# Kernel tuning notes

Measured on AMD Instinct MI355X. Metric: run time of the kernel, lower is better.

The kernel has to match this reference:

```python
import jax, jax.numpy as jnp
import numpy as np

N_ACTIVE = 200000
N_IN = 64
N_OUT = 64
K = 27          # filter volume (3^3)
R = 100000      # rulebook pairs per filter offset


def setup_inputs() -> dict:
    key = jax.random.key(0)
    k1, k2, k3, k4 = jax.random.split(key, 4)
    std = (2.0 / (N_IN * K)) ** 0.5
    features = jax.random.normal(k1, (N_ACTIVE, N_IN), dtype=jnp.float32)
    weight = jax.random.normal(k2, (N_IN * K, N_OUT), dtype=jnp.float32) * std
    bias = jnp.zeros((N_OUT,), dtype=jnp.float32)
    in_idx = jax.random.randint(k3, (K, R), 0, N_ACTIVE, dtype=jnp.int64 if jax.config.jax_enable_x64 else jnp.int32)
    out_idx = jax.random.randint(k4, (K, R), 0, N_ACTIVE, dtype=jnp.int64 if jax.config.jax_enable_x64 else jnp.int32)
    return {"features": features, "weight": weight, "bias": bias,
            "in_idx": in_idx, "out_idx": out_idx}


def reference(features, weight, bias, in_idx, out_idx):
    # Rulebook-based submanifold sparse convolution:
    # for each filter offset k: gather inputs, matmul with weight slice,
    # scatter-accumulate into output sites. Bias added once per active site.
    n_active, n_in = features.shape
    k = in_idx.shape[0]
    W = weight.reshape(k, n_in, -1)            # [K, nIn, nOut]
    gathered = features[in_idx]                # [K, R, nIn]  (irregular gather)
    contrib = jnp.einsum('kri,kio->kro', gathered, W)  # grouped matmul
    out = jnp.zeros((n_active, W.shape[2]), dtype=features.dtype)
    out = out.at[out_idx.reshape(-1)].add(contrib.reshape(-1, W.shape[2]))
    return out + bias
```

## Files before the change

kernel.cpp:

```cpp
#include <hip/hip_runtime.h>
#include <stdint.h>

#define N_ACTIVE 200000
#define N_IN 64
#define N_OUT 64
#define K_FILT 27
#define R_PAIRS 100000
#define TOTP (K_FILT * R_PAIRS)
#define NSLOT (N_ACTIVE * K_FILT)

#define CF_BLOCKS (N_ACTIVE * N_IN / 8 / 256)
#define CW_BLOCKS K_FILT
#define CL_BLOCKS ((TOTP + 255) / 256)

typedef __bf16 bf16x8 __attribute__((ext_vector_type(8)));
typedef float f32x4 __attribute__((ext_vector_type(4)));

__global__ __launch_bounds__(256) void prep_fused(
    const float* __restrict__ feat, __bf16* __restrict__ featb,
    const float* __restrict__ wsrc, __bf16* __restrict__ wt,
    const int* __restrict__ in_idx, const int* __restrict__ out_idx,
    int* __restrict__ slotW,
    int2* __restrict__ ovf, int* __restrict__ ovfCur)
{
    int bb = blockIdx.x, t = threadIdx.x;
    if (bb < CF_BLOCKS) {
        int i = bb * 256 + t;
        const f32x4* src = reinterpret_cast<const f32x4*>(feat) + 2 * (size_t)i;
        f32x4 v0 = __builtin_nontemporal_load(src);
        f32x4 v1 = __builtin_nontemporal_load(src + 1);
        bf16x8 o;
        o[0] = (__bf16)v0[0]; o[1] = (__bf16)v0[1]; o[2] = (__bf16)v0[2]; o[3] = (__bf16)v0[3];
        o[4] = (__bf16)v1[0]; o[5] = (__bf16)v1[1]; o[6] = (__bf16)v1[2]; o[7] = (__bf16)v1[3];
        reinterpret_cast<bf16x8*>(featb)[i] = o;
    } else if (bb < CF_BLOCKS + CW_BLOCKS) {
        int kf = bb - CF_BLOCKS;
        const float* wk = wsrc + kf * 4096;
        __bf16* wo = wt + kf * 4096;
        int o = t >> 2, i0 = (t & 3) * 16;
        bf16x8 a, b;
        #pragma unroll
        for (int j = 0; j < 8; ++j) a[j] = (__bf16)wk[(i0 + j) * 64 + o];
        #pragma unroll
        for (int j = 0; j < 8; ++j) b[j] = (__bf16)wk[(i0 + 8 + j) * 64 + o];
        *reinterpret_cast<bf16x8*>(wo + o * 64 + i0) = a;
        *reinterpret_cast<bf16x8*>(wo + o * 64 + i0 + 8) = b;
    } else {
        int p = (bb - CF_BLOCKS - CW_BLOCKS) * 256 + t;
        if (p < TOTP) {
            unsigned k = (unsigned)p / (unsigned)R_PAIRS;
            int row = out_idx[p];
            int iv  = in_idx[p];
            int slot = row * K_FILT + (int)k;
            int c = atomicAdd(&slotW[slot * 4], 1);
            if (c < 3) slotW[slot * 4 + 1 + c] = iv;
            else {
                int q = atomicAdd(ovfCur, 1);
                ovf[q] = make_int2(slot, iv);
            }
        }
    }
}

__global__ __launch_bounds__(256, 4) void conv_slots(
    const __bf16* __restrict__ featb,
    const __bf16* __restrict__ wtb,
    const float* __restrict__ bias,
    const int4* __restrict__ slotT,
    float* __restrict__ out)
{
    const int t = threadIdx.x;
    const int w = t >> 6;
    const int lane = t & 63;
    const int lrow = lane & 15;
    const int kg   = lane >> 4;
    const int kgo  = kg * 8;
    const int rowBase = blockIdx.x * 64 + w * 16;
    const int slotBase = (rowBase + lrow) * K_FILT;

    f32x4 acc0 = {0.f,0.f,0.f,0.f}, acc1 = acc0, acc2 = acc0, acc3 = acc0;
    const float b0 = bias[lrow], b1 = bias[16 + lrow],
                b2 = bias[32 + lrow], b3 = bias[48 + lrow];
    const bf16x8 zero8 = {};

    #pragma unroll 9
    for (int kf = 0; kf < K_FILT; ++kf) {
        int4 sv = slotT[slotBase + kf];
        int c  = sv.x;
        int a1 = (c > 0) ? sv.y : 0;
        int a2 = (c > 1) ? sv.z : 0;
        int a3 = (c > 2) ? sv.w : 0;

        const __bf16* p1 = featb + (size_t)a1 * 64 + kgo;
        const __bf16* p2 = featb + (size_t)a2 * 64 + kgo;
        const __bf16* p3 = featb + (size_t)a3 * 64 + kgo;
        bf16x8 x0 = *reinterpret_cast<const bf16x8*>(p1);
        bf16x8 x1 = *reinterpret_cast<const bf16x8*>(p1 + 32);
        bf16x8 y0 = *reinterpret_cast<const bf16x8*>(p2);
        bf16x8 y1 = *reinterpret_cast<const bf16x8*>(p2 + 32);
        bf16x8 z0 = *reinterpret_cast<const bf16x8*>(p3);
        bf16x8 z1 = *reinterpret_cast<const bf16x8*>(p3 + 32);

        const __bf16* wk = wtb + kf * 4096;
        bf16x8 bf00 = *reinterpret_cast<const bf16x8*>(wk + (lrow)      * 64 + kgo);
        bf16x8 bf01 = *reinterpret_cast<const bf16x8*>(wk + (lrow)      * 64 + 32 + kgo);
        bf16x8 bf10 = *reinterpret_cast<const bf16x8*>(wk + (16 + lrow) * 64 + kgo);
        bf16x8 bf11 = *reinterpret_cast<const bf16x8*>(wk + (16 + lrow) * 64 + 32 + kgo);
        bf16x8 bf20 = *reinterpret_cast<const bf16x8*>(wk + (32 + lrow) * 64 + kgo);
        bf16x8 bf21 = *reinterpret_cast<const bf16x8*>(wk + (32 + lrow) * 64 + 32 + kgo);
        bf16x8 bf30 = *reinterpret_cast<const bf16x8*>(wk + (48 + lrow) * 64 + kgo);
        bf16x8 bf31 = *reinterpret_cast<const bf16x8*>(wk + (48 + lrow) * 64 + 32 + kgo);

        x0 = (c > 0) ? x0 : zero8;  x1 = (c > 0) ? x1 : zero8;
        y0 = (c > 1) ? y0 : zero8;  y1 = (c > 1) ? y1 : zero8;
        z0 = (c > 2) ? z0 : zero8;  z1 = (c > 2) ? z1 : zero8;
        bf16x8 A0, A1;
        #pragma unroll
        for (int j = 0; j < 8; ++j) {
            float f0 = (float)x0[j] + (float)y0[j] + (float)z0[j];
            float f1 = (float)x1[j] + (float)y1[j] + (float)z1[j];
            A0[j] = (__bf16)f0;
            A1[j] = (__bf16)f1;
        }

        acc0 = __builtin_amdgcn_mfma_f32_16x16x32_bf16(A0, bf00, acc0, 0, 0, 0);
        acc0 = __builtin_amdgcn_mfma_f32_16x16x32_bf16(A1, bf01, acc0, 0, 0, 0);
        acc1 = __builtin_amdgcn_mfma_f32_16x16x32_bf16(A0, bf10, acc1, 0, 0, 0);
        acc1 = __builtin_amdgcn_mfma_f32_16x16x32_bf16(A1, bf11, acc1, 0, 0, 0);
        acc2 = __builtin_amdgcn_mfma_f32_16x16x32_bf16(A0, bf20, acc2, 0, 0, 0);
        acc2 = __builtin_amdgcn_mfma_f32_16x16x32_bf16(A1, bf21, acc2, 0, 0, 0);
        acc3 = __builtin_amdgcn_mfma_f32_16x16x32_bf16(A0, bf30, acc3, 0, 0, 0);
        acc3 = __builtin_amdgcn_mfma_f32_16x16x32_bf16(A1, bf31, acc3, 0, 0, 0);
    }

    #pragma unroll
    for (int r = 0; r < 4; ++r) {
        int gr = rowBase + kg * 4 + r;
        float* orow = out + (size_t)gr * 64;
        __builtin_nontemporal_store(acc0[r] + b0, &orow[lrow]);
        __builtin_nontemporal_store(acc1[r] + b1, &orow[16 + lrow]);
        __builtin_nontemporal_store(acc2[r] + b2, &orow[32 + lrow]);
        __builtin_nontemporal_store(acc3[r] + b3, &orow[48 + lrow]);
    }
}

__global__ __launch_bounds__(64) void ovf_cleanup(
    const __bf16* __restrict__ featb, const __bf16* __restrict__ wtb,
    const int2* __restrict__ ovf, const int* __restrict__ ovfCur,
    float* __restrict__ out)
{
    const int n = *ovfCur;
    const int lane = threadIdx.x;
    for (int e = blockIdx.x; e < n; e += gridDim.x) {
        int2 v = ovf[e];
        int slot = v.x, in = v.y;
        int row = slot / K_FILT;
        int kf  = slot - row * K_FILT;
        const __bf16* fp = featb + (size_t)in * 64;
        const __bf16* wp = wtb + kf * 4096 + lane * 64;
        float s = 0.f;
        #pragma unroll
        for (int j = 0; j < 8; ++j) {
            bf16x8 fv = *reinterpret_cast<const bf16x8*>(fp + j * 8);
            bf16x8 wv = *reinterpret_cast<const bf16x8*>(wp + j * 8);
            #pragma unroll
            for (int q = 0; q < 8; ++q) s += (float)fv[q] * (float)wv[q];
        }
        atomicAdd(&out[(size_t)row * 64 + lane], s);
    }
}

extern "C" void kernel_launch(void* const* d_in, const int* in_sizes, int n_in,
                              void* d_out, int out_size, void* d_ws, size_t ws_size,
                              hipStream_t stream) {
    const float* feat    = (const float*)d_in[0];
    const float* weight  = (const float*)d_in[1];
    const float* bias    = (const float*)d_in[2];
    const int*   in_idx  = (const int*)d_in[3];
    const int*   out_idx = (const int*)d_in[4];
    float* out = (float*)d_out;

    char* wsb = (char*)d_ws;
    __bf16* featb  = (__bf16*)wsb;
    __bf16* wtb    = (__bf16*)(wsb + 25600000);
    int*  slotW    = (int*) (wsb + 25600000 + 221184);
    int*  ovfCur   = slotW + (size_t)NSLOT * 4;
    int2* ovf      = (int2*)(ovfCur + 4);

    hipMemsetAsync(slotW, 0, (size_t)NSLOT * 16, stream);
    hipMemsetAsync(ovfCur, 0, 16, stream);

    prep_fused<<<dim3(CF_BLOCKS + CW_BLOCKS + CL_BLOCKS), dim3(256), 0, stream>>>(
        feat, featb, weight, wtb, in_idx, out_idx, slotW, ovf, ovfCur);
    conv_slots<<<dim3(N_ACTIVE / 64), dim3(256), 0, stream>>>(
        featb, wtb, bias, (const int4*)slotW, out);
    ovf_cleanup<<<dim3(2048), dim3(64), 0, stream>>>(featb, wtb, ovf, ovfCur, out);
}
```

Before: 627.1 us.

## Pack slot table to 8 bytes with count in high bits, stage in LDS

The slot table shrinks from four ints to two per slot. The count lives in the top bits of the first word, alongside the first input index, and a second word holds the second index; further entries spill to the overflow list. The conv kernel stages its block's slot table in shared memory and issues the second-neighbour gather only when some lane in the wave has more than one entry. This halves the memset and table traffic and skips most second and third gathers. In exchange, more entries fall to the slower atomic overflow path, and the packing assumes indices fit in 18 bits.

```diff
diff --git a/kernel.cpp b/kernel.cpp
--- a/kernel.cpp
+++ b/kernel.cpp
@@ -52,8 +52,10 @@
             int row = out_idx[p];
             int iv  = in_idx[p];
             int slot = row * K_FILT + (int)k;
-            int c = atomicAdd(&slotW[slot * 4], 1);
-            if (c < 3) slotW[slot * 4 + 1 + c] = iv;
+            int old = atomicAdd(&slotW[slot * 2], 1 << 18);
+            int c = old >> 18;
+            if (c == 0)      atomicOr(&slotW[slot * 2], iv);
+            else if (c == 1) slotW[slot * 2 + 1] = iv;
             else {
                 int q = atomicAdd(ovfCur, 1);
                 ovf[q] = make_int2(slot, iv);
@@ -66,9 +68,11 @@
     const __bf16* __restrict__ featb,
     const __bf16* __restrict__ wtb,
     const float* __restrict__ bias,
-    const int4* __restrict__ slotT,
+    const int2* __restrict__ slotP,
     float* __restrict__ out)
 {
+    __shared__ int2 sTab[64 * K_FILT];
+
     const int t = threadIdx.x;
     const int w = t >> 6;
     const int lane = t & 63;
@@ -76,30 +80,33 @@
     const int kg   = lane >> 4;
     const int kgo  = kg * 8;
     const int rowBase = blockIdx.x * 64 + w * 16;
-    const int slotBase = (rowBase + lrow) * K_FILT;
+
+    {
+        const int4* src = reinterpret_cast<const int4*>(slotP + (size_t)blockIdx.x * (64 * K_FILT));
+        int4* dst = reinterpret_cast<int4*>(sTab);
+        #pragma unroll
+        for (int j = 0; j < 4; ++j) {
+            int i = j * 256 + t;
+            if (i < 864) dst[i] = src[i];
+        }
+    }
+    __syncthreads();
+
+    const int2* myRow = sTab + (w * 16 + lrow) * K_FILT;
 
     f32x4 acc0 = {0.f,0.f,0.f,0.f}, acc1 = acc0, acc2 = acc0, acc3 = acc0;
     const float b0 = bias[lrow], b1 = bias[16 + lrow],
                 b2 = bias[32 + lrow], b3 = bias[48 + lrow];
     const bf16x8 zero8 = {};
 
-    #pragma unroll 9
     for (int kf = 0; kf < K_FILT; ++kf) {
-        int4 sv = slotT[slotBase + kf];
-        int c  = sv.x;
-        int a1 = (c > 0) ? sv.y : 0;
-        int a2 = (c > 1) ? sv.z : 0;
-        int a3 = (c > 2) ? sv.w : 0;
+        int2 sv = myRow[kf];
+        int c  = ((unsigned)sv.x) >> 18;
+        int a1 = (c > 0) ? (sv.x & 0x3FFFF) : 0;
 
         const __bf16* p1 = featb + (size_t)a1 * 64 + kgo;
-        const __bf16* p2 = featb + (size_t)a2 * 64 + kgo;
-        const __bf16* p3 = featb + (size_t)a3 * 64 + kgo;
         bf16x8 x0 = *reinterpret_cast<const bf16x8*>(p1);
         bf16x8 x1 = *reinterpret_cast<const bf16x8*>(p1 + 32);
-        bf16x8 y0 = *reinterpret_cast<const bf16x8*>(p2);
-        bf16x8 y1 = *reinterpret_cast<const bf16x8*>(p2 + 32);
-        bf16x8 z0 = *reinterpret_cast<const bf16x8*>(p3);
-        bf16x8 z1 = *reinterpret_cast<const bf16x8*>(p3 + 32);
 
         const __bf16* wk = wtb + kf * 4096;
         bf16x8 bf00 = *reinterpret_cast<const bf16x8*>(wk + (lrow)      * 64 + kgo);
@@ -111,16 +118,21 @@
         bf16x8 bf30 = *reinterpret_cast<const bf16x8*>(wk + (48 + lrow) * 64 + kgo);
         bf16x8 bf31 = *reinterpret_cast<const bf16x8*>(wk + (48 + lrow) * 64 + 32 + kgo);
 
-        x0 = (c > 0) ? x0 : zero8;  x1 = (c > 0) ? x1 : zero8;
-        y0 = (c > 1) ? y0 : zero8;  y1 = (c > 1) ? y1 : zero8;
-        z0 = (c > 2) ? z0 : zero8;  z1 = (c > 2) ? z1 : zero8;
-        bf16x8 A0, A1;
-        #pragma unroll
-        for (int j = 0; j < 8; ++j) {
-            float f0 = (float)x0[j] + (float)y0[j] + (float)z0[j];
-            float f1 = (float)x1[j] + (float)y1[j] + (float)z1[j];
-            A0[j] = (__bf16)f0;
-            A1[j] = (__bf16)f1;
+        bf16x8 A0 = (c > 0) ? x0 : zero8;
+        bf16x8 A1 = (c > 0) ? x1 : zero8;
+
+        if (__any(c > 1)) {
+            int a2 = (c > 1) ? sv.y : a1;
+            const __bf16* p2 = featb + (size_t)a2 * 64 + kgo;
+            bf16x8 y0 = *reinterpret_cast<const bf16x8*>(p2);
+            bf16x8 y1 = *reinterpret_cast<const bf16x8*>(p2 + 32);
+            y0 = (c > 1) ? y0 : zero8;
+            y1 = (c > 1) ? y1 : zero8;
+            #pragma unroll
+            for (int j = 0; j < 8; ++j) {
+                A0[j] = (__bf16)((float)A0[j] + (float)y0[j]);
+                A1[j] = (__bf16)((float)A1[j] + (float)y1[j]);
+            }
         }
 
         acc0 = __builtin_amdgcn_mfma_f32_16x16x32_bf16(A0, bf00, acc0, 0, 0, 0);
@@ -184,15 +196,15 @@
     __bf16* featb  = (__bf16*)wsb;
     __bf16* wtb    = (__bf16*)(wsb + 25600000);
     int*  slotW    = (int*) (wsb + 25600000 + 221184);
-    int*  ovfCur   = slotW + (size_t)NSLOT * 4;
+    int*  ovfCur   = slotW + (size_t)NSLOT * 2;
     int2* ovf      = (int2*)(ovfCur + 4);
 
-    hipMemsetAsync(slotW, 0, (size_t)NSLOT * 16, stream);
+    hipMemsetAsync(slotW, 0, (size_t)NSLOT * 8, stream);
     hipMemsetAsync(ovfCur, 0, 16, stream);
 
     prep_fused<<<dim3(CF_BLOCKS + CW_BLOCKS + CL_BLOCKS), dim3(256), 0, stream>>>(
         feat, featb, weight, wtb, in_idx, out_idx, slotW, ovf, ovfCur);
     conv_slots<<<dim3(N_ACTIVE / 64), dim3(256), 0, stream>>>(
-        featb, wtb, bias, (const int4*)slotW, out);
+        featb, wtb, bias, (const int2*)slotW, out);
     ovf_cleanup<<<dim3(2048), dim3(64), 0, stream>>>(featb, wtb, ovf, ovfCur, out);
 }
```

Result: slower. 889.9 us (+41.9%).

## Stage slot table in LDS, prefetch next gather, skip secondary gathers wave-uniformly

Applied to the files above, without the earlier changes.

The conv kernel now copies the block's slot table into shared memory up front and reads slot entries from LDS. It software-pipelines the first-neighbour feature gather one filter offset ahead. The second and third gathers, plus the bf16 summation, run only when some lane in the wave has more than one pair for that slot. The goal is to cut wasted global loads and hide gather latency, at the cost of extra LDS, a block barrier, loop unrolling removed, and more live registers.

```diff
diff --git a/kernel.cpp b/kernel.cpp
--- a/kernel.cpp
+++ b/kernel.cpp
@@ -69,6 +69,8 @@
     const int4* __restrict__ slotT,
     float* __restrict__ out)
 {
+    __shared__ int4 sTab[64 * K_FILT];
+
     const int t = threadIdx.x;
     const int w = t >> 6;
     const int lane = t & 63;
@@ -76,30 +78,41 @@
     const int kg   = lane >> 4;
     const int kgo  = kg * 8;
     const int rowBase = blockIdx.x * 64 + w * 16;
-    const int slotBase = (rowBase + lrow) * K_FILT;
+
+    {
+        const int4* src = slotT + (size_t)blockIdx.x * (64 * K_FILT);
+        #pragma unroll
+        for (int j = 0; j < 7; ++j) {
+            int i = j * 256 + t;
+            if (i < 64 * K_FILT) sTab[i] = src[i];
+        }
+    }
+    __syncthreads();
+
+    const int4* myRow = sTab + (w * 16 + lrow) * K_FILT;
 
     f32x4 acc0 = {0.f,0.f,0.f,0.f}, acc1 = acc0, acc2 = acc0, acc3 = acc0;
     const float b0 = bias[lrow], b1 = bias[16 + lrow],
                 b2 = bias[32 + lrow], b3 = bias[48 + lrow];
     const bf16x8 zero8 = {};
 
-    #pragma unroll 9
+    int4 sv = myRow[0];
+    {
+        int a1 = (sv.x > 0) ? sv.y : 0;
+        (void)a1;
+    }
+    int a1c = (sv.x > 0) ? sv.y : 0;
+    const __bf16* p1c = featb + (size_t)a1c * 64 + kgo;
+    bf16x8 x0 = *reinterpret_cast<const bf16x8*>(p1c);
+    bf16x8 x1 = *reinterpret_cast<const bf16x8*>(p1c + 32);
+
     for (int kf = 0; kf < K_FILT; ++kf) {
-        int4 sv = slotT[slotBase + kf];
-        int c  = sv.x;
-        int a1 = (c > 0) ? sv.y : 0;
-        int a2 = (c > 1) ? sv.z : 0;
-        int a3 = (c > 2) ? sv.w : 0;
-
-        const __bf16* p1 = featb + (size_t)a1 * 64 + kgo;
-        const __bf16* p2 = featb + (size_t)a2 * 64 + kgo;
-        const __bf16* p3 = featb + (size_t)a3 * 64 + kgo;
-        bf16x8 x0 = *reinterpret_cast<const bf16x8*>(p1);
-        bf16x8 x1 = *reinterpret_cast<const bf16x8*>(p1 + 32);
-        bf16x8 y0 = *reinterpret_cast<const bf16x8*>(p2);
-        bf16x8 y1 = *reinterpret_cast<const bf16x8*>(p2 + 32);
-        bf16x8 z0 = *reinterpret_cast<const bf16x8*>(p3);
-        bf16x8 z1 = *reinterpret_cast<const bf16x8*>(p3 + 32);
+        int nk = (kf + 1 < K_FILT) ? kf + 1 : K_FILT - 1;
+        int4 svn = myRow[nk];
+        int a1n = (svn.x > 0) ? svn.y : 0;
+        const __bf16* p1n = featb + (size_t)a1n * 64 + kgo;
+        bf16x8 nx0 = *reinterpret_cast<const bf16x8*>(p1n);
+        bf16x8 nx1 = *reinterpret_cast<const bf16x8*>(p1n + 32);
 
         const __bf16* wk = wtb + kf * 4096;
         bf16x8 bf00 = *reinterpret_cast<const bf16x8*>(wk + (lrow)      * 64 + kgo);
@@ -111,16 +124,26 @@
         bf16x8 bf30 = *reinterpret_cast<const bf16x8*>(wk + (48 + lrow) * 64 + kgo);
         bf16x8 bf31 = *reinterpret_cast<const bf16x8*>(wk + (48 + lrow) * 64 + 32 + kgo);
 
-        x0 = (c > 0) ? x0 : zero8;  x1 = (c > 0) ? x1 : zero8;
-        y0 = (c > 1) ? y0 : zero8;  y1 = (c > 1) ? y1 : zero8;
-        z0 = (c > 2) ? z0 : zero8;  z1 = (c > 2) ? z1 : zero8;
-        bf16x8 A0, A1;
-        #pragma unroll
-        for (int j = 0; j < 8; ++j) {
-            float f0 = (float)x0[j] + (float)y0[j] + (float)z0[j];
-            float f1 = (float)x1[j] + (float)y1[j] + (float)z1[j];
-            A0[j] = (__bf16)f0;
-            A1[j] = (__bf16)f1;
+        int c = sv.x;
+        bf16x8 A0 = (c > 0) ? x0 : zero8;
+        bf16x8 A1 = (c > 0) ? x1 : zero8;
+
+        if (__any(c > 1)) {
+            int a2 = (c > 1) ? sv.z : a1c;
+            int a3 = (c > 2) ? sv.w : a1c;
+            const __bf16* p2 = featb + (size_t)a2 * 64 + kgo;
+            const __bf16* p3 = featb + (size_t)a3 * 64 + kgo;
+            bf16x8 y0 = *reinterpret_cast<const bf16x8*>(p2);
+            bf16x8 y1 = *reinterpret_cast<const bf16x8*>(p2 + 32);
+            bf16x8 z0 = *reinterpret_cast<const bf16x8*>(p3);
+            bf16x8 z1 = *reinterpret_cast<const bf16x8*>(p3 + 32);
+            y0 = (c > 1) ? y0 : zero8;  y1 = (c > 1) ? y1 : zero8;
+            z0 = (c > 2) ? z0 : zero8;  z1 = (c > 2) ? z1 : zero8;
+            #pragma unroll
+            for (int j = 0; j < 8; ++j) {
+                A0[j] = (__bf16)((float)A0[j] + (float)y0[j] + (float)z0[j]);
+                A1[j] = (__bf16)((float)A1[j] + (float)y1[j] + (float)z1[j]);
+            }
         }
 
         acc0 = __builtin_amdgcn_mfma_f32_16x16x32_bf16(A0, bf00, acc0, 0, 0, 0);
@@ -131,6 +154,8 @@
         acc2 = __builtin_amdgcn_mfma_f32_16x16x32_bf16(A1, bf21, acc2, 0, 0, 0);
         acc3 = __builtin_amdgcn_mfma_f32_16x16x32_bf16(A0, bf30, acc3, 0, 0, 0);
         acc3 = __builtin_amdgcn_mfma_f32_16x16x32_bf16(A1, bf31, acc3, 0, 0, 0);
+
+        sv = svn; a1c = a1n; x0 = nx0; x1 = nx1;
     }
 
     #pragma unroll
```

Measured after the change: 645.8 us. 1.03x slower.
